# Kernel optimization log

Measured on AMD Instinct MI355X. Metric: run time of the kernel, lower is better.

## Reference

```python
import jax, jax.numpy as jnp
import numpy as np

D_IN, D_H, BATCH = 4096, 512, 8192


def _layernorm(x, g, b, eps=1e-5):
    mu = jnp.mean(x, axis=-1, keepdims=True)
    var = jnp.var(x, axis=-1, keepdims=True)
    return (x - mu) * jax.lax.rsqrt(var + eps) * g + b


def setup_inputs() -> dict:
    key = jax.random.key(0)
    ks = jax.random.split(key, 10)
    x = jax.random.normal(ks[0], (BATCH, D_IN), jnp.float32)
    h = jax.random.normal(ks[1], (BATCH, D_H), jnp.float32)
    s1 = 1.0 / np.sqrt(D_IN + D_H)
    W1 = jax.random.uniform(ks[2], (D_IN + D_H, D_H), jnp.float32, -s1, s1)
    b1 = jnp.zeros((D_H,), jnp.float32)
    ln1_g = jnp.ones((D_H,), jnp.float32)
    ln1_b = jnp.zeros((D_H,), jnp.float32)
    s2 = 1.0 / np.sqrt(D_H)
    W2 = jax.random.uniform(ks[3], (D_H, 3 * D_H), jnp.float32, -s2, s2)
    b2 = jnp.zeros((3 * D_H,), jnp.float32)
    base_tau = jnp.ones((D_H,), jnp.float32)  # time_constant_init = 1.0
    base_A = jax.random.normal(ks[4], (D_H, D_H), jnp.float32) * 0.1
    idx = jnp.arange(D_H)
    base_A = base_A.at[idx, idx].set(-0.5)
    base_B = jax.random.normal(ks[5], (D_IN, D_H), jnp.float32) * 0.1
    hn_g = jnp.ones((D_H,), jnp.float32)
    hn_b = jnp.zeros((D_H,), jnp.float32)
    return {"x": x, "h": h, "W1": W1, "b1": b1, "ln1_g": ln1_g, "ln1_b": ln1_b,
            "W2": W2, "b2": b2, "base_tau": base_tau, "base_A": base_A,
            "base_B": base_B, "hn_g": hn_g, "hn_b": hn_b}


def reference(x, h, W1, b1, ln1_g, ln1_b, W2, b2, base_tau, base_A, base_B, hn_g, hn_b):
    dt = 0.1
    # time_net hypernetwork
    xh = jnp.concatenate([x, h], axis=-1)                 # [B, D_IN+D_H]
    t = _layernorm(xh @ W1 + b1, ln1_g, ln1_b)
    t = jax.nn.gelu(t, approximate=False)
    params = t @ W2 + b2                                  # [B, 3*D_H]
    tau_s, A_s, B_s = jnp.split(params, 3, axis=-1)
    tau = base_tau * (jax.nn.sigmoid(tau_s) * 2.0)        # [B, D_H]
    A_row = 1.0 + 0.5 * jnp.tanh(A_s)                     # per-sample row scale of A
    B_col = 1.0 + 0.5 * jnp.tanh(B_s)                     # per-sample col scale of B
    # A[b] = base_A * A_row[b][:,None]; h @ A[b].T == (h @ base_A.T) * A_row[b]
    recurrent = (h @ base_A.T) * A_row                    # [B, D_H]
    # B[b] = base_B * B_col[b][None,:]; x @ B[b] == (x @ base_B) * B_col[b]
    input_term = (x @ base_B) * B_col                     # [B, D_H]
    dhdt = -h / (tau + 1e-8) + jnp.tanh(recurrent + input_term)
    new_h = _layernorm(h + dt * dhdt, hn_g, hn_b)
    return new_h
```

## Files before the change

kernel.cpp:

```cpp
#include <hip/hip_runtime.h>

#define BATCH 8192
#define DIN 4096
#define DH 512

typedef float f32x4 __attribute__((ext_vector_type(4)));
typedef float f32x2 __attribute__((ext_vector_type(2)));
typedef short s16x8 __attribute__((ext_vector_type(8)));
typedef unsigned short u16x2 __attribute__((ext_vector_type(2)));
typedef unsigned short u16x4 __attribute__((ext_vector_type(4)));
typedef unsigned short u16x8 __attribute__((ext_vector_type(8)));

static __device__ __forceinline__ unsigned short f2bf(float f) {
  unsigned int u = __float_as_uint(f);
  u += 0x7FFFu + ((u >> 16) & 1u);
  return (unsigned short)(u >> 16);
}
static __device__ __forceinline__ float bf2f(unsigned short s) {
  return __uint_as_float(((unsigned int)s) << 16);
}

typedef const __attribute__((address_space(1))) unsigned int* gas_ptr;
typedef __attribute__((address_space(3))) unsigned int* las_ptr;
static __device__ __forceinline__ void gl_lds16(const unsigned short* g, unsigned short* l) {
  __builtin_amdgcn_global_load_lds((gas_ptr)g, (las_ptr)l, 16, 0, 0);
}

__global__ __launch_bounds__(256) void cast_bf16_k(
    const float* __restrict__ in, unsigned short* __restrict__ out)
{
  const int i = (blockIdx.x * 256 + threadIdx.x) * 4;
  f32x4 v = *(const f32x4*)(in + i);
  u16x4 p = { f2bf(v[0]), f2bf(v[1]), f2bf(v[2]), f2bf(v[3]) };
  *(u16x4*)(out + i) = p;
}

__global__ __launch_bounds__(256) void transpose_bf16_k(
    const float* __restrict__ in, int R, int C,
    unsigned short* __restrict__ out, int ldo, int row_off)
{
  __shared__ float tl[32][33];
  const int tx = threadIdx.x, ty = threadIdx.y;
  const int c0 = blockIdx.x * 32, r0 = blockIdx.y * 32;
#pragma unroll
  for (int i = 0; i < 4; i++)
    tl[ty + 8 * i][tx] = in[(size_t)(r0 + ty + 8 * i) * C + c0 + tx];
  __syncthreads();
#pragma unroll
  for (int i = 0; i < 4; i++)
    out[(size_t)(row_off + c0 + ty + 8 * i) * ldo + r0 + tx] = f2bf(tl[tx][ty + 8 * i]);
}

__global__ __launch_bounds__(256) void zfill_k(
    unsigned short* __restrict__ base, int ld, int rows, int cols8)
{
  const int gid = blockIdx.x * 256 + threadIdx.x;
  const int row = gid / cols8;
  const int c = (gid % cols8) * 8;
  if (row < rows) {
    u16x8 z = { 0, 0, 0, 0, 0, 0, 0, 0 };
    *(u16x8*)(base + (size_t)row * ld + c) = z;
  }
}

template<int EPI, bool SWZ>
__global__ __launch_bounds__(256) void gemm_lds_k(
    const unsigned short* __restrict__ A0, int lda0, int K0,
    const unsigned short* __restrict__ A1, int lda1, int K1,
    const unsigned short* __restrict__ BT, int ldb,
    unsigned short* __restrict__ C0, int ldc,
    unsigned short* __restrict__ C1,
    const float* __restrict__ bias,
    const float* __restrict__ base_tau)
{
  __shared__ unsigned short Asm_[128][32];
  __shared__ unsigned short Bsm_[128][32];

  const int tid = threadIdx.x;
  const int lane = tid & 63;
  const int wid = tid >> 6;
  const int wm = (wid >> 1) * 64;
  const int wn = (wid & 1) * 64;

  int virt;
  if (SWZ) {
    const int cpx = gridDim.x >> 3;
    virt = (blockIdx.x & 7) * cpx + (blockIdx.x >> 3);
  } else {
    virt = blockIdx.x;
  }
  const int by = virt & 63;
  const int bx = virt >> 6;
  const int mb = by * 128;
  const int nb = bx * 128;
  const int K = K0 + K1;

  f32x4 acc[4][4];
#pragma unroll
  for (int i = 0; i < 4; i++)
#pragma unroll
    for (int j = 0; j < 4; j++)
      acc[i][j] = (f32x4){ 0.f, 0.f, 0.f, 0.f };

  const int srow = lane >> 2;
  const int scol = (lane & 3) * 8;
  const int fr = lane & 15;
  const int fk = (lane >> 4) * 8;

  for (int k0 = 0; k0 < K; k0 += 32) {
    const bool s0 = (k0 < K0);
    const unsigned short* Ab = s0 ? A0 : A1;
    const int ld = s0 ? lda0 : lda1;
    const int ko = (s0 ? k0 : k0 - K0) + scol;
#pragma unroll
    for (int c = 0; c < 2; c++) {
      const int r = 32 * wid + c * 16 + srow;
      gl_lds16(Ab + (size_t)(mb + r) * ld + ko, &Asm_[32 * wid + c * 16][0]);
      gl_lds16(BT + (size_t)(nb + r) * ldb + k0 + scol, &Bsm_[32 * wid + c * 16][0]);
    }
    __syncthreads();

    s16x8 af[4], bfv[4];
#pragma unroll
    for (int mi = 0; mi < 4; mi++)
      af[mi] = *(const s16x8*)&Asm_[wm + mi * 16 + fr][fk];
#pragma unroll
    for (int ni = 0; ni < 4; ni++)
      bfv[ni] = *(const s16x8*)&Bsm_[wn + ni * 16 + fr][fk];
#pragma unroll
    for (int mi = 0; mi < 4; mi++)
#pragma unroll
      for (int ni = 0; ni < 4; ni++)
        acc[mi][ni] = __builtin_amdgcn_mfma_f32_16x16x32_bf16(
            af[mi], bfv[ni], acc[mi][ni], 0, 0, 0);
    __syncthreads();
  }

  const int rb = (lane >> 4) * 4;
#pragma unroll
  for (int mi = 0; mi < 4; mi++) {
#pragma unroll
    for (int ni = 0; ni < 4; ni++) {
#pragma unroll
      for (int r = 0; r < 4; r++) {
        const int row = mb + wm + mi * 16 + rb + r;
        const int col = nb + wn + ni * 16 + fr;
        float v = acc[mi][ni][r];
        if (EPI == 3) {
          if (col < DH) C0[(size_t)row * DH + col] = f2bf(v + bias[col]);
          else          C1[(size_t)row * DH + (col - DH)] = f2bf(v);
        } else if (EPI == 2) {
          C0[(size_t)row * ldc + col] = f2bf(v);
        } else if (EPI == 1) {
          v += bias[col];
          if ((col >> 9) == 0) {
            const float s = 1.0f / (1.0f + expf(-v));
            v = 1.0f / (base_tau[col & (DH - 1)] * 2.0f * s + 1e-8f);
          } else {
            v = 1.0f + 0.5f * tanhf(v);
          }
          C0[(size_t)row * ldc + col] = f2bf(v);
        }
      }
    }
  }
}

__device__ __forceinline__ float block_sum256(float v, float* red) {
#pragma unroll
  for (int m = 32; m >= 1; m >>= 1) v += __shfl_xor(v, m, 64);
  __syncthreads();
  if ((threadIdx.x & 63) == 0) red[threadIdx.x >> 6] = v;
  __syncthreads();
  return red[0] + red[1] + red[2] + red[3];
}

__global__ __launch_bounds__(256) void ln_gelu_k(
    const unsigned short* __restrict__ pre,
    const float* __restrict__ g, const float* __restrict__ b,
    unsigned short* __restrict__ t)
{
  __shared__ float red[4];
  const int row = blockIdx.x;
  const int c = threadIdx.x * 2;
  const size_t ro = (size_t)row * DH;
  u16x2 raw = *(const u16x2*)(pre + ro + c);
  const float v0 = bf2f(raw[0]), v1 = bf2f(raw[1]);
  const float mu = block_sum256(v0 + v1, red) * (1.0f / DH);
  const float d0 = v0 - mu, d1 = v1 - mu;
  const float var = block_sum256(d0 * d0 + d1 * d1, red) * (1.0f / DH);
  const float inv = rsqrtf(var + 1e-5f);
  const float y0 = d0 * inv * g[c] + b[c];
  const float y1 = d1 * inv * g[c + 1] + b[c + 1];
  u16x2 o = { f2bf(0.5f * y0 * (1.0f + erff(y0 * 0.70710678118f))),
              f2bf(0.5f * y1 * (1.0f + erff(y1 * 0.70710678118f))) };
  *(u16x2*)(t + ro + c) = o;
}

__global__ __launch_bounds__(256) void final_k(
    const float* __restrict__ h,
    const unsigned short* __restrict__ rawA,
    const unsigned short* __restrict__ rawB,
    const unsigned short* __restrict__ scales,
    const float* __restrict__ hn_g, const float* __restrict__ hn_b,
    float* __restrict__ out)
{
  __shared__ float red[4];
  const int row = blockIdx.x;
  const int c = threadIdx.x * 2;
  const size_t ro = (size_t)row * DH;
  f32x2 hv = *(const f32x2*)(h + ro + c);
  u16x2 ra = *(const u16x2*)(rawA + ro + c);
  u16x2 rb = *(const u16x2*)(rawB + ro + c);
  const unsigned short* sc = scales + (size_t)row * (3 * DH);
  u16x2 ti  = *(const u16x2*)(sc + c);
  u16x2 arw = *(const u16x2*)(sc + DH + c);
  u16x2 bcl = *(const u16x2*)(sc + 2 * DH + c);
  const float u0 = hv[0] + 0.1f * (-hv[0] * bf2f(ti[0])
                 + tanhf(bf2f(ra[0]) * bf2f(arw[0]) + bf2f(rb[0]) * bf2f(bcl[0])));
  const float u1 = hv[1] + 0.1f * (-hv[1] * bf2f(ti[1])
                 + tanhf(bf2f(ra[1]) * bf2f(arw[1]) + bf2f(rb[1]) * bf2f(bcl[1])));
  const float mu = block_sum256(u0 + u1, red) * (1.0f / DH);
  const float d0 = u0 - mu, d1 = u1 - mu;
  const float var = block_sum256(d0 * d0 + d1 * d1, red) * (1.0f / DH);
  const float inv = rsqrtf(var + 1e-5f);
  f32x2 o = { d0 * inv * hn_g[c] + hn_b[c],
              d1 * inv * hn_g[c + 1] + hn_b[c + 1] };
  *(f32x2*)(out + ro + c) = o;
}

extern "C" void kernel_launch(void* const* d_in, const int* in_sizes, int n_in,
                              void* d_out, int out_size, void* d_ws, size_t ws_size,
                              hipStream_t stream)
{
  const float* x        = (const float*)d_in[0];
  const float* h        = (const float*)d_in[1];
  const float* W1       = (const float*)d_in[2];
  const float* b1       = (const float*)d_in[3];
  const float* ln1_g    = (const float*)d_in[4];
  const float* ln1_b    = (const float*)d_in[5];
  const float* W2       = (const float*)d_in[6];
  const float* b2       = (const float*)d_in[7];
  const float* base_tau = (const float*)d_in[8];
  const float* base_A   = (const float*)d_in[9];
  const float* base_B   = (const float*)d_in[10];
  const float* hn_g     = (const float*)d_in[11];
  const float* hn_b     = (const float*)d_in[12];

  const int KC = DIN + DH;
  char* w = (char*)d_ws;
  unsigned short* xbf    = (unsigned short*)(w);
  unsigned short* hbf    = (unsigned short*)(w + 67108864);
  unsigned short* BTcat  = (unsigned short*)(w + 75497472);
  unsigned short* tbf    = (unsigned short*)(w + 75497472);
  unsigned short* W2T    = (unsigned short*)(w + 84934656);
  unsigned short* Abf    = (unsigned short*)(w + 86507520);
  unsigned short* pre1   = (unsigned short*)(w + 87031808);
  unsigned short* rawA   = (unsigned short*)(w + 87031808);
  unsigned short* rawB   = (unsigned short*)(w + 95420416);
  unsigned short* scales = (unsigned short*)(w + 103809024);

  cast_bf16_k<<<DIN * BATCH / 1024, 256, 0, stream>>>(x, xbf);
  cast_bf16_k<<<DH * BATCH / 1024, 256, 0, stream>>>(h, hbf);
  cast_bf16_k<<<DH * DH / 1024, 256, 0, stream>>>(base_A, Abf);
  dim3 tb(32, 8);
  transpose_bf16_k<<<dim3(DH / 32, KC / 32), tb, 0, stream>>>(W1, KC, DH, BTcat, KC, 0);
  transpose_bf16_k<<<dim3(DH / 32, DIN / 32), tb, 0, stream>>>(base_B, DIN, DH, BTcat, KC, DH);
  zfill_k<<<128, 256, 0, stream>>>(BTcat + (size_t)DH * KC + DIN, KC, DH, DH / 8);
  transpose_bf16_k<<<dim3(3 * DH / 32, DH / 32), tb, 0, stream>>>(W2, DH, 3 * DH, W2T, DH, 0);

  gemm_lds_k<3, true><<<512, 256, 0, stream>>>(
      xbf, DIN, DIN, hbf, DH, DH, BTcat, KC, pre1, DH, rawB, b1, nullptr);
  ln_gelu_k<<<BATCH, 256, 0, stream>>>(pre1, ln1_g, ln1_b, tbf);
  gemm_lds_k<2, false><<<256, 256, 0, stream>>>(
      hbf, DH, DH, nullptr, 0, 0, Abf, DH, rawA, DH, nullptr, nullptr, nullptr);
  gemm_lds_k<1, false><<<768, 256, 0, stream>>>(
      tbf, DH, DH, nullptr, 0, 0, W2T, DH, scales, 3 * DH, nullptr, b2, base_tau);
  final_k<<<BATCH, 256, 0, stream>>>(h, rawA, rawB, scales, hn_g, hn_b, (float*)d_out);
}
```

Baseline: 263.9 us.

## Triple-buffer GEMM LDS loads with async prefetch and merge tail GEMMs

Refactors the bf16 MFMA GEMM into a shared engine that uses a three-stage LDS ring. Tiles are prefetched two iterations ahead, with explicit vmcnt waits and a single barrier per step replacing the two syncthreads. The aim is to overlap global-to-LDS loads with MFMA work in the large K=4608 GEMM. It also merges the h@A and t@W2 GEMMs into one 1024-block launch to save a launch and fill the device better. The ring triples LDS use per block, which may reduce occupancy, and the hand-placed waitcnt counts must stay correct.

```diff
diff --git a/kernel.cpp b/kernel.cpp
--- a/kernel.cpp
+++ b/kernel.cpp
@@ -63,77 +63,88 @@
   }
 }
 
-template<int EPI, bool SWZ>
-__global__ __launch_bounds__(256) void gemm_lds_k(
+template<int EPI>
+static __device__ __forceinline__ void gemm_engine(
     const unsigned short* __restrict__ A0, int lda0, int K0,
-    const unsigned short* __restrict__ A1, int lda1, int K1,
+    const unsigned short* __restrict__ A1, int lda1,
     const unsigned short* __restrict__ BT, int ldb,
     unsigned short* __restrict__ C0, int ldc,
     unsigned short* __restrict__ C1,
     const float* __restrict__ bias,
-    const float* __restrict__ base_tau)
-{
-  __shared__ unsigned short Asm_[128][32];
-  __shared__ unsigned short Bsm_[128][32];
-
+    const float* __restrict__ base_tau,
+    int mb, int nb, int K,
+    unsigned short* As, unsigned short* Bs)
+{
   const int tid = threadIdx.x;
   const int lane = tid & 63;
   const int wid = tid >> 6;
   const int wm = (wid >> 1) * 64;
   const int wn = (wid & 1) * 64;
-
-  int virt;
-  if (SWZ) {
-    const int cpx = gridDim.x >> 3;
-    virt = (blockIdx.x & 7) * cpx + (blockIdx.x >> 3);
-  } else {
-    virt = blockIdx.x;
-  }
-  const int by = virt & 63;
-  const int bx = virt >> 6;
-  const int mb = by * 128;
-  const int nb = bx * 128;
-  const int K = K0 + K1;
-
-  f32x4 acc[4][4];
-#pragma unroll
-  for (int i = 0; i < 4; i++)
-#pragma unroll
-    for (int j = 0; j < 4; j++)
-      acc[i][j] = (f32x4){ 0.f, 0.f, 0.f, 0.f };
-
   const int srow = lane >> 2;
   const int scol = (lane & 3) * 8;
   const int fr = lane & 15;
   const int fk = (lane >> 4) * 8;
-
-  for (int k0 = 0; k0 < K; k0 += 32) {
+  const int NT = K / 32;
+
+  f32x4 acc[4][4];
+#pragma unroll
+  for (int i = 0; i < 4; i++)
+#pragma unroll
+    for (int j = 0; j < 4; j++)
+      acc[i][j] = (f32x4){ 0.f, 0.f, 0.f, 0.f };
+
+  auto STAGE = [&](int buf, int t) {
+    const int k0 = t * 32;
     const bool s0 = (k0 < K0);
     const unsigned short* Ab = s0 ? A0 : A1;
     const int ld = s0 ? lda0 : lda1;
     const int ko = (s0 ? k0 : k0 - K0) + scol;
+    unsigned short* ab = As + buf * 4096 + (32 * wid) * 32;
+    unsigned short* bb = Bs + buf * 4096 + (32 * wid) * 32;
 #pragma unroll
     for (int c = 0; c < 2; c++) {
       const int r = 32 * wid + c * 16 + srow;
-      gl_lds16(Ab + (size_t)(mb + r) * ld + ko, &Asm_[32 * wid + c * 16][0]);
-      gl_lds16(BT + (size_t)(nb + r) * ldb + k0 + scol, &Bsm_[32 * wid + c * 16][0]);
+      gl_lds16(Ab + (size_t)(mb + r) * ld + ko, ab + c * 16 * 32);
+      gl_lds16(BT + (size_t)(nb + r) * ldb + k0 + scol, bb + c * 16 * 32);
     }
-    __syncthreads();
-
-    s16x8 af[4], bfv[4];
+  };
+
+  STAGE(0, 0);
+  STAGE(1, 1);
+  asm volatile("s_waitcnt vmcnt(4)" ::: "memory");
+  __builtin_amdgcn_s_barrier();
+
+  int cur = 0, stg = 2;
+  for (int t = 0; t < NT; t++) {
+    if (t + 2 < NT) STAGE(stg, t + 2);
+
+    const unsigned short* ar = As + cur * 4096;
+    const unsigned short* br = Bs + cur * 4096;
+    s16x8 af[4], bv[4];
 #pragma unroll
     for (int mi = 0; mi < 4; mi++)
-      af[mi] = *(const s16x8*)&Asm_[wm + mi * 16 + fr][fk];
+      af[mi] = *(const s16x8*)(ar + (wm + mi * 16 + fr) * 32 + fk);
 #pragma unroll
     for (int ni = 0; ni < 4; ni++)
-      bfv[ni] = *(const s16x8*)&Bsm_[wn + ni * 16 + fr][fk];
+      bv[ni] = *(const s16x8*)(br + (wn + ni * 16 + fr) * 32 + fk);
+
+    asm volatile("s_waitcnt lgkmcnt(0)" ::: "memory");
+    __builtin_amdgcn_sched_barrier(0);
+
 #pragma unroll
     for (int mi = 0; mi < 4; mi++)
 #pragma unroll
       for (int ni = 0; ni < 4; ni++)
         acc[mi][ni] = __builtin_amdgcn_mfma_f32_16x16x32_bf16(
-            af[mi], bfv[ni], acc[mi][ni], 0, 0, 0);
-    __syncthreads();
+            af[mi], bv[ni], acc[mi][ni], 0, 0, 0);
+
+    if (t + 1 < NT) {
+      if (t + 2 < NT) asm volatile("s_waitcnt vmcnt(4)" ::: "memory");
+      else            asm volatile("s_waitcnt vmcnt(0)" ::: "memory");
+      __builtin_amdgcn_s_barrier();
+    }
+    cur = (cur == 2) ? 0 : cur + 1;
+    stg = (stg == 2) ? 0 : stg + 1;
   }
 
   const int rb = (lane >> 4) * 4;
@@ -166,6 +177,49 @@
   }
 }
 
+__global__ __launch_bounds__(256) void fused_gemm_k(
+    const unsigned short* __restrict__ xbf,
+    const unsigned short* __restrict__ hbf,
+    const unsigned short* __restrict__ BTcat,
+    unsigned short* __restrict__ pre1,
+    unsigned short* __restrict__ rawB,
+    const float* __restrict__ b1)
+{
+  __shared__ unsigned short As[3 * 4096];
+  __shared__ unsigned short Bs[3 * 4096];
+  const int cpx = gridDim.x >> 3;
+  const int virt = (blockIdx.x & 7) * cpx + (blockIdx.x >> 3);
+  const int mb = (virt & 63) * 128;
+  const int nb = (virt >> 6) * 128;
+  gemm_engine<3>(xbf, DIN, DIN, hbf, DH, BTcat, DIN + DH,
+                 pre1, DH, rawB, b1, nullptr, mb, nb, DIN + DH, As, Bs);
+}
+
+__global__ __launch_bounds__(256) void tail_gemm_k(
+    const unsigned short* __restrict__ hbf,
+    const unsigned short* __restrict__ Abf,
+    const unsigned short* __restrict__ tbf,
+    const unsigned short* __restrict__ W2T,
+    unsigned short* __restrict__ rawA,
+    unsigned short* __restrict__ scales,
+    const float* __restrict__ b2,
+    const float* __restrict__ base_tau)
+{
+  __shared__ unsigned short As[3 * 4096];
+  __shared__ unsigned short Bs[3 * 4096];
+  const int b = blockIdx.x;
+  if (b < 768) {
+    const int mb = (b & 63) * 128, nb = (b >> 6) * 128;
+    gemm_engine<1>(tbf, DH, DH, nullptr, 0, W2T, DH,
+                   scales, 3 * DH, nullptr, b2, base_tau, mb, nb, DH, As, Bs);
+  } else {
+    const int b2i = b - 768;
+    const int mb = (b2i & 63) * 128, nb = (b2i >> 6) * 128;
+    gemm_engine<2>(hbf, DH, DH, nullptr, 0, Abf, DH,
+                   rawA, DH, nullptr, nullptr, nullptr, mb, nb, DH, As, Bs);
+  }
+}
+
 __device__ __forceinline__ float block_sum256(float v, float* red) {
 #pragma unroll
   for (int m = 32; m >= 1; m >>= 1) v += __shfl_xor(v, m, 64);
@@ -269,12 +323,8 @@
   zfill_k<<<128, 256, 0, stream>>>(BTcat + (size_t)DH * KC + DIN, KC, DH, DH / 8);
   transpose_bf16_k<<<dim3(3 * DH / 32, DH / 32), tb, 0, stream>>>(W2, DH, 3 * DH, W2T, DH, 0);
 
-  gemm_lds_k<3, true><<<512, 256, 0, stream>>>(
-      xbf, DIN, DIN, hbf, DH, DH, BTcat, KC, pre1, DH, rawB, b1, nullptr);
+  fused_gemm_k<<<512, 256, 0, stream>>>(xbf, hbf, BTcat, pre1, rawB, b1);
   ln_gelu_k<<<BATCH, 256, 0, stream>>>(pre1, ln1_g, ln1_b, tbf);
-  gemm_lds_k<2, false><<<256, 256, 0, stream>>>(
-      hbf, DH, DH, nullptr, 0, 0, Abf, DH, rawA, DH, nullptr, nullptr, nullptr);
-  gemm_lds_k<1, false><<<768, 256, 0, stream>>>(
-      tbf, DH, DH, nullptr, 0, 0, W2T, DH, scales, 3 * DH, nullptr, b2, base_tau);
+  tail_gemm_k<<<1024, 256, 0, stream>>>(hbf, Abf, tbf, W2T, rawA, scales, b2, base_tau);
   final_k<<<BATCH, 256, 0, stream>>>(h, rawA, rawB, scales, hn_g, hn_b, (float*)d_out);
 }
```

Result: faster. 242.0 us (-8.3%).
